# Kernel optimization log

Hardware: AMD Instinct MI355X
Metric: run time of the kernel (lower is better)

The kernel has to match this reference:

```python
import jax, jax.numpy as jnp
import numpy as np

IN_DIM, OUT_DIM, HID = 32, 1, 256
H0, H1, H2 = HID // 4, HID // 2, HID
B, S = 256, 512


def setup_inputs() -> dict:
    key = jax.random.key(0)
    ks = jax.random.split(key, 16)

    def u(k, shape, fan):
        bound = 1.0 / np.sqrt(fan)
        return jax.random.uniform(k, shape, jnp.float32, -bound, bound)

    inp = {"noise": jax.random.normal(ks[0], (B, S, IN_DIM), jnp.float32)}
    dims = [(IN_DIM, H0), (H0, H1), (H1, H2)]
    for i, (din, h) in enumerate(dims):
        inp[f"Wih{i}"] = u(ks[1 + 4 * i], (4 * h, din), h)  # torch gate order i,f,g,o
        inp[f"Whh{i}"] = u(ks[2 + 4 * i], (4 * h, h), h)
        inp[f"bih{i}"] = u(ks[3 + 4 * i], (4 * h,), h)
        inp[f"bhh{i}"] = u(ks[4 + 4 * i], (4 * h,), h)
    inp["Wl"] = u(ks[13], (OUT_DIM, H2), H2)
    inp["bl"] = u(ks[14], (OUT_DIM,), H2)
    return inp


def lstm_layer(x, Wih, Whh, bih, bhh):
    # x: [B, S, D] -> hidden sequence [B, S, H]; zero initial (h, c), torch gate order i,f,g,o
    Bb = x.shape[0]
    H = Whh.shape[1]
    pre = jnp.einsum('bsd,gd->bsg', x, Wih) + bih + bhh  # input GEMM for all timesteps at once

    def step(carry, pre_t):
        h, c = carry
        g = pre_t + h @ Whh.T  # [B, 4H]
        i, f, gg, o = jnp.split(g, 4, axis=-1)
        c = jax.nn.sigmoid(f) * c + jax.nn.sigmoid(i) * jnp.tanh(gg)
        h = jax.nn.sigmoid(o) * jnp.tanh(c)
        return (h, c), h

    h0 = jnp.zeros((Bb, H), x.dtype)
    c0 = jnp.zeros((Bb, H), x.dtype)
    _, hs = jax.lax.scan(step, (h0, c0), jnp.swapaxes(pre, 0, 1))  # scan over time
    return jnp.swapaxes(hs, 0, 1)


def reference(noise, Wih0, Whh0, bih0, bhh0, Wih1, Whh1, bih1, bhh1,
              Wih2, Whh2, bih2, bhh2, Wl, bl):
    x = lstm_layer(noise, Wih0, Whh0, bih0, bhh0)   # [B, S, 64]
    x = lstm_layer(x, Wih1, Whh1, bih1, bhh1)        # [B, S, 128]
    x = lstm_layer(x, Wih2, Whh2, bih2, bhh2)        # [B, S, 256]
    return jnp.tanh(jnp.einsum('bsh,oh->bso', x, Wl) + bl)  # [B, S, OUT_DIM]
```

## Files before the change

kernel.cpp:

```cpp
#include <hip/hip_runtime.h>
#include <hip/hip_fp16.h>

#define DEVINL __device__ __forceinline__

constexpr int B = 256, S = 512;
constexpr int H0 = 64, H1 = 128, H2 = 256;

typedef _Float16 f16x8 __attribute__((ext_vector_type(8)));
typedef float f32x4 __attribute__((ext_vector_type(4)));
typedef _Float16 h2v __attribute__((ext_vector_type(2)));

DEVINL float fexp2(float x) { return __builtin_amdgcn_exp2f(x); }
DEVINL float frcp(float x) { return __builtin_amdgcn_rcpf(x); }
DEVINL float fsig(float x) { return frcp(1.f + fexp2(-1.44269504088896f * x)); }
DEVINL float ftanh_(float x) { return 1.f - 2.f * frcp(1.f + fexp2(2.88539008177793f * x)); }
DEVINL h2v as_h2(unsigned u) { union { unsigned u; h2v h; } x; x.u = u; return x.h; }
DEVINL float fdot2(unsigned a, unsigned b, float c) {
  return __builtin_amdgcn_fdot2(as_h2(a), as_h2(b), c, false);
}
union FU { uint4 u; f16x8 h; };
DEVINL f16x8 as_f16x8(uint4 u) { FU x; x.u = u; return x.h; }

DEVINL unsigned long long agldull(unsigned long long* p) {
  return __hip_atomic_load(p, __ATOMIC_RELAXED, __HIP_MEMORY_SCOPE_AGENT);
}
DEVINL void agstull(unsigned long long* p, unsigned long long v) {
  __hip_atomic_store(p, v, __ATOMIC_RELAXED, __HIP_MEMORY_SCOPE_AGENT);
}


__global__ __launch_bounds__(256) void pack_frag(const float* __restrict__ w,
    uint4* __restrict__ wp, int Hch, int Kdim, int MT, int KT) {
  int o = blockIdx.x * 256 + threadIdx.x;
  if (o >= MT * KT * 64) return;
  int lane = o & 63, fk = o >> 6;
  int kt = fk % KT, mt = fk / KT;
  int rp = mt * 16 + (lane & 15);
  int orig = (rp & 3) * Hch + (rp >> 2);
  int k0 = kt * 32 + (lane >> 4) * 8;
  unsigned r[4];
#pragma unroll
  for (int p = 0; p < 4; ++p) {
    unsigned lo = __half_as_ushort(__float2half_rn(w[(size_t)orig * Kdim + k0 + 2 * p]));
    unsigned hi = __half_as_ushort(__float2half_rn(w[(size_t)orig * Kdim + k0 + 2 * p + 1]));
    r[p] = lo | (hi << 16);
  }
  uint4 v; v.x = r[0]; v.y = r[1]; v.z = r[2]; v.w = r[3];
  wp[o] = v;
}

__global__ __launch_bounds__(256) void pack_bias(const float* __restrict__ bih,
    const float* __restrict__ bhh, float* __restrict__ bs, int Hch) {
  int rp = blockIdx.x * 256 + threadIdx.x;
  if (rp >= 4 * Hch) return;
  int orig = (rp & 3) * Hch + (rp >> 2);
  bs[rp] = bih[orig] + bhh[orig];
}

__global__ void pack_wl(const float* __restrict__ wl, unsigned* __restrict__ wlp, int n) {
  int i = threadIdx.x;
  if (i < n) {
    unsigned lo = __half_as_ushort(__float2half_rn(wl[2 * i]));
    unsigned hi = __half_as_ushort(__float2half_rn(wl[2 * i + 1]));
    wlp[i] = lo | (hi << 16);
  }
}

__global__ __launch_bounds__(256) void f2h(const float* __restrict__ x,
                                           __half* __restrict__ y, int n8) {
  int i = blockIdx.x * 256 + threadIdx.x;
  if (i >= n8) return;
  float4 a = *(const float4*)(x + i * 8);
  float4 b = *(const float4*)(x + i * 8 + 4);
  __half h[8];
  h[0] = __float2half_rn(a.x); h[1] = __float2half_rn(a.y);
  h[2] = __float2half_rn(a.z); h[3] = __float2half_rn(a.w);
  h[4] = __float2half_rn(b.x); h[5] = __float2half_rn(b.y);
  h[6] = __float2half_rn(b.z); h[7] = __float2half_rn(b.w);
  *(uint4*)(y + i * 8) = *(const uint4*)h;
}

#define KBLK(BUF, K0, K1)                                                           \
  _Pragma("unroll") for (int kt = (K0); kt < (K1); ++kt) {                          \
    f16x8 bfrag = as_f16x8(*(const uint4*)((BUF) + n16 * HP + kt * 32 + quad * 8)); \
    _Pragma("unroll") for (int im = 0; im < MTW; ++im)                              \
      acc[im] = __builtin_amdgcn_mfma_f32_16x16x32_f16(                             \
          as_f16x8(areg[im][kt]), bfrag, acc[im], 0, 0, 0);                         \
  }

template <int H, int SPLIT, bool FINAL, int KTI>
DEVINL void scan_body(
    int bx, const __half* x, const uint4* wpI, const float* bs,
    const uint4* wp, f32x4* preT, __half* xout, float* out,
    const unsigned* wlp, const float* blp,
    float* sth, float* stc, unsigned long long* xh,
    int Sc, int t0, int first) {
  constexpr int MT = H / 4;
  constexpr int MTO = MT / SPLIT;
  constexpr int MTW = MTO / 8;
  constexpr int KT = H / 32;
  constexpr int HP = H + 8;
  constexpr int CH_OWN = MTO * 4;

  __shared__ __half hb[2][16 * HP];
  __shared__ unsigned wls[FINAL ? H / 2 : 1];

  const int tid = threadIdx.x, w = tid >> 6, lane = tid & 63;
  const int n16 = lane & 15, quad = lane >> 4;
  int bt, half;
  if constexpr (SPLIT == 2) { bt = bx & 15; half = bx >> 4; }
  else { bt = bx; half = 0; }
  const int b0 = bt * 16;
  const int mbase = half * MTO;

  {
    constexpr int KI = KTI * 32;
    uint4 wih[MTW][KTI];
#pragma unroll
    for (int im = 0; im < MTW; ++im)
#pragma unroll
      for (int kt = 0; kt < KTI; ++kt)
        wih[im][kt] = wpI[((size_t)(mbase + w * MTW + im) * KTI + kt) * 64 + lane];
    f32x4 bini[MTW];
#pragma unroll
    for (int im = 0; im < MTW; ++im)
      bini[im] = *(const f32x4*)(bs + (mbase + w * MTW + im) * 16 + quad * 4);
    uint4 bfr[KTI];
    {
      const __half* xr = x + ((size_t)(b0 + n16) * S + t0) * KI + quad * 8;
#pragma unroll
      for (int kt = 0; kt < KTI; ++kt) bfr[kt] = *(const uint4*)(xr + kt * 32);
    }
    for (int t = 0; t < Sc; ++t) {
      uint4 cur[KTI];
#pragma unroll
      for (int kt = 0; kt < KTI; ++kt) cur[kt] = bfr[kt];
      if (t + 1 < Sc) {
        const __half* xr = x + ((size_t)(b0 + n16) * S + t0 + t + 1) * KI + quad * 8;
#pragma unroll
        for (int kt = 0; kt < KTI; ++kt) bfr[kt] = *(const uint4*)(xr + kt * 32);
      }
      f32x4 ac[MTW];
#pragma unroll
      for (int im = 0; im < MTW; ++im) ac[im] = bini[im];
#pragma unroll
      for (int kt = 0; kt < KTI; ++kt)
#pragma unroll
        for (int im = 0; im < MTW; ++im)
          ac[im] = __builtin_amdgcn_mfma_f32_16x16x32_f16(as_f16x8(wih[im][kt]),
                                                          as_f16x8(cur[kt]), ac[im], 0, 0, 0);
#pragma unroll
      for (int im = 0; im < MTW; ++im)
        preT[((size_t)(bt * Sc + t) * MT + mbase + w * MTW + im) * 64 + lane] = ac[im];
    }
  }
  asm volatile("s_waitcnt vmcnt(0)" ::: "memory");

  uint4 areg[MTW][KT];
#pragma unroll
  for (int im = 0; im < MTW; ++im)
#pragma unroll
    for (int kt = 0; kt < KT; ++kt)
      areg[im][kt] = wp[((size_t)(mbase + w * MTW + im) * KT + kt) * 64 + lane];

  if constexpr (FINAL)
    for (int i = tid; i < H / 2; i += 512) wls[i] = wlp[i];

  float cst[MTW];
#pragma unroll
  for (int im = 0; im < MTW; ++im) {
    int ch = (mbase + w * MTW + im) * 4 + quad;
    cst[im] = first ? 0.f : stc[(size_t)(b0 + n16) * H + ch];
  }
  for (int i = tid; i < 16 * H; i += 512) {
    int n = i / H, ch = i % H;
    hb[0][n * HP + ch] = first ? __float2half_rn(0.f)
                               : __float2half_rn(sth[(size_t)(b0 + n) * H + ch]);
  }
  __syncthreads();

  const float bl0 = FINAL ? blp[0] : 0.f;

  auto emit_out = [&](const __half* rbuf, int t_out) {
    if constexpr (FINAL) {
      if ((SPLIT == 1 || half == 0) && tid < 128) {
        int n = tid >> 3, seg = tid & 7;
        const unsigned* hrow = (const unsigned*)(rbuf + n * HP);
        float s = 0.f;
#pragma unroll
        for (int p = 0; p < 16; ++p) s = fdot2(hrow[seg * 16 + p], wls[seg * 16 + p], s);
        s += __shfl_xor(s, 1); s += __shfl_xor(s, 2); s += __shfl_xor(s, 4);
        if (seg == 0) out[(size_t)(b0 + n) * S + t_out] = ftanh_(s + bl0);
      }
    } else {
      if (tid < 16 * (H / 8)) {
        int n = tid / (H / 8), kq = tid % (H / 8);
        uint4 v = *(const uint4*)(rbuf + n * HP + kq * 8);
        *(uint4*)(xout + ((size_t)(b0 + n) * S + t_out) * H + kq * 8) = v;
      }
    }
  };

  f32x4 nxt[MTW];
#pragma unroll
  for (int im = 0; im < MTW; ++im)
    nxt[im] = preT[((size_t)(bt * Sc) * MT + mbase + w * MTW + im) * 64 + lane];

  for (int tl = 0; tl < Sc; ++tl) {
    __half* rb = hb[tl & 1];
    __half* wb = hb[(tl + 1) & 1];
    f32x4 acc[MTW];
#pragma unroll
    for (int im = 0; im < MTW; ++im) acc[im] = nxt[im];
    if (tl + 1 < Sc) {
#pragma unroll
      for (int im = 0; im < MTW; ++im)
        nxt[im] = preT[((size_t)(bt * Sc + tl + 1) * MT + mbase + w * MTW + im) * 64 + lane];
    }

    if constexpr (SPLIT == 2) {
      unsigned long long v0 = 0, v1 = 0;
      unsigned long long* src = nullptr;
      const unsigned seq = (unsigned)(t0 + tl);
      const int j0 = w * 128 + lane;
      if (tl > 0) {
        src = xh + (((size_t)((t0 + tl - 1) & 1) * 16 + bt) * 2 + (1 - half)) * 1024;
        v0 = agldull(src + j0);
        v1 = agldull(src + j0 + 64);
      }
      if (half == 0) { KBLK(rb, 0, KT / 2) } else { KBLK(rb, KT / 2, KT) }
      if (tl > 0) {
        for (;;) {
          bool ok = ((unsigned)(v0 >> 32) == seq) & ((unsigned)(v1 >> 32) == seq);
          if (__all(ok)) break;
          __builtin_amdgcn_s_sleep(1);
          v0 = agldull(src + j0);
          v1 = agldull(src + j0 + 64);
        }
        int c0 = j0 >> 3, dn0 = j0 & 7;
        rb[(2 * dn0) * HP + (1 - half) * CH_OWN + c0] =
            __ushort_as_half((unsigned short)(v0 & 0xffffu));
        rb[(2 * dn0 + 1) * HP + (1 - half) * CH_OWN + c0] =
            __ushort_as_half((unsigned short)((v0 >> 16) & 0xffffu));
        int j1 = j0 + 64, c1 = j1 >> 3, dn1 = j1 & 7;
        rb[(2 * dn1) * HP + (1 - half) * CH_OWN + c1] =
            __ushort_as_half((unsigned short)(v1 & 0xffffu));
        rb[(2 * dn1 + 1) * HP + (1 - half) * CH_OWN + c1] =
            __ushort_as_half((unsigned short)((v1 >> 16) & 0xffffu));
        __syncthreads();
      }
      if (half == 0) { KBLK(rb, KT / 2, KT) } else { KBLK(rb, 0, KT / 2) }
      if (tl > 0) emit_out(rb, t0 + tl - 1);
    } else {
      if (tl > 0) emit_out(rb, t0 + tl - 1);
      KBLK(rb, 0, KT)
    }

    __half hh[MTW];
#pragma unroll
    for (int im = 0; im < MTW; ++im) {
      float gi = fsig(acc[im][0]);
      float gf = fsig(acc[im][1]);
      float gg = ftanh_(acc[im][2]);
      float go = fsig(acc[im][3]);
      float cn = gf * cst[im] + gi * gg;
      cst[im] = cn;
      hh[im] = __float2half_rn(go * ftanh_(cn));
    }

    if constexpr (SPLIT == 2) {
      const int hid = t0 + tl;
      const unsigned eseq = (unsigned)(hid + 1);
      unsigned long long* dst =
          xh + (((size_t)(hid & 1) * 16 + bt) * 2 + half) * 1024;
#pragma unroll
      for (int im = 0; im < MTW; ++im) {
        unsigned m = (unsigned)__half_as_ushort(hh[im]);
        unsigned o = (unsigned)__shfl_xor((int)m, 1);
        if (!(lane & 1)) {
          int cl = (w * MTW + im) * 4 + quad;
          agstull(dst + cl * 8 + (n16 >> 1),
                  ((unsigned long long)eseq << 32) | (unsigned long long)(m | (o << 16)));
        }
      }
#pragma unroll
      for (int im = 0; im < MTW; ++im)
        wb[n16 * HP + (mbase + w * MTW + im) * 4 + quad] = hh[im];
      __syncthreads();
    } else {
#pragma unroll
      for (int im = 0; im < MTW; ++im)
        wb[n16 * HP + (mbase + w * MTW + im) * 4 + quad] = hh[im];
      __syncthreads();
    }
  }

  __half* fb = hb[Sc & 1];
  if constexpr (SPLIT == 2) {
    const unsigned seq = (unsigned)(t0 + Sc);
    unsigned long long* src =
        xh + (((size_t)((t0 + Sc - 1) & 1) * 16 + bt) * 2 + (1 - half)) * 1024;
    const int j0 = w * 128 + lane;
    unsigned long long v0 = agldull(src + j0), v1 = agldull(src + j0 + 64);
    for (;;) {
      bool ok = ((unsigned)(v0 >> 32) == seq) & ((unsigned)(v1 >> 32) == seq);
      if (__all(ok)) break;
      __builtin_amdgcn_s_sleep(1);
      v0 = agldull(src + j0);
      v1 = agldull(src + j0 + 64);
    }
    int c0 = j0 >> 3, dn0 = j0 & 7;
    fb[(2 * dn0) * HP + (1 - half) * CH_OWN + c0] =
        __ushort_as_half((unsigned short)(v0 & 0xffffu));
    fb[(2 * dn0 + 1) * HP + (1 - half) * CH_OWN + c0] =
        __ushort_as_half((unsigned short)((v0 >> 16) & 0xffffu));
    int j1 = j0 + 64, c1 = j1 >> 3, dn1 = j1 & 7;
    fb[(2 * dn1) * HP + (1 - half) * CH_OWN + c1] =
        __ushort_as_half((unsigned short)(v1 & 0xffffu));
    fb[(2 * dn1 + 1) * HP + (1 - half) * CH_OWN + c1] =
        __ushort_as_half((unsigned short)((v1 >> 16) & 0xffffu));
    __syncthreads();
  }

  emit_out(fb, t0 + Sc - 1);

  for (int i = tid; i < 16 * H; i += 512) {
    int n = i / H, ch = i % H;
    sth[(size_t)(b0 + n) * H + ch] = __half2float(fb[n * HP + ch]);
  }
#pragma unroll
  for (int im = 0; im < MTW; ++im) {
    int ch = (mbase + w * MTW + im) * 4 + quad;
    stc[(size_t)(b0 + n16) * H + ch] = cst[im];
  }
}
#undef KBLK

__global__ __launch_bounds__(512) void scan_fat(
    const __half* x0, __half* x1, __half* x2,
    const uint4* wpI0, const uint4* wpI1, const uint4* wpI2,
    const float* bs0, const float* bs1, const float* bs2,
    const uint4* wpH0, const uint4* wpH1, const uint4* wpH2,
    f32x4* preT0, f32x4* preT1, f32x4* preT2,
    float* out, const unsigned* wlp, const float* blp,
    float* sh0, float* sc0, float* sh1, float* sc1, float* sh2, float* sc2,
    unsigned long long* xh, int Sc, int slot, int NC) {
  int b = blockIdx.x;
  if (b < 16) {
    int c = slot;
    if (c >= NC) return;
    scan_body<64, 1, false, 1>(b, x0, wpI0, bs0, wpH0, preT0, x1, nullptr,
                               nullptr, nullptr, sh0, sc0, nullptr, Sc, c * Sc, c == 0);
  } else if (b < 32) {
    int c = slot - 1;
    if (c < 0 || c >= NC) return;
    scan_body<128, 1, false, 2>(b - 16, x1, wpI1, bs1, wpH1, preT1, x2, nullptr,
                                nullptr, nullptr, sh1, sc1, nullptr, Sc, c * Sc, c == 0);
  } else {
    int c = slot - 2;
    if (c < 0 || c >= NC) return;
    scan_body<256, 2, true, 4>(b - 32, x2, wpI2, bs2, wpH2, preT2, nullptr, out,
                               wlp, blp, sh2, sc2, xh, Sc, c * Sc, c == 0);
  }
}

extern "C" void kernel_launch(void* const* d_in, const int* in_sizes, int n_in,
                              void* d_out, int out_size, void* d_ws, size_t ws_size,
                              hipStream_t stream) {
  (void)in_sizes; (void)n_in; (void)out_size;
  const float* noise = (const float*)d_in[0];
  const float* Wih0 = (const float*)d_in[1];
  const float* Whh0 = (const float*)d_in[2];
  const float* bih0 = (const float*)d_in[3];
  const float* bhh0 = (const float*)d_in[4];
  const float* Wih1 = (const float*)d_in[5];
  const float* Whh1 = (const float*)d_in[6];
  const float* bih1 = (const float*)d_in[7];
  const float* bhh1 = (const float*)d_in[8];
  const float* Wih2 = (const float*)d_in[9];
  const float* Whh2 = (const float*)d_in[10];
  const float* bih2 = (const float*)d_in[11];
  const float* bhh2 = (const float*)d_in[12];
  const float* Wl = (const float*)d_in[13];
  const float* bl = (const float*)d_in[14];
  float* out = (float*)d_out;

  char* p = (char*)d_ws;
  auto alloc = [&](size_t bytes) {
    char* r = p;
    p += (bytes + 255) & ~(size_t)255;
    return r;
  };
  uint4* wpH0 = (uint4*)alloc((size_t)16 * 2 * 1024);
  uint4* wpH1 = (uint4*)alloc((size_t)32 * 4 * 1024);
  uint4* wpH2 = (uint4*)alloc((size_t)64 * 8 * 1024);
  uint4* wpI0 = (uint4*)alloc((size_t)16 * 1 * 1024);
  uint4* wpI1 = (uint4*)alloc((size_t)32 * 2 * 1024);
  uint4* wpI2 = (uint4*)alloc((size_t)64 * 4 * 1024);
  float* bs0 = (float*)alloc(256 * 4);
  float* bs1 = (float*)alloc(512 * 4);
  float* bs2 = (float*)alloc(1024 * 4);
  unsigned* wlp = (unsigned*)alloc(128 * 4);
  float* sh0 = (float*)alloc((size_t)B * H0 * 4);
  float* sc0 = (float*)alloc((size_t)B * H0 * 4);
  float* sh1 = (float*)alloc((size_t)B * H1 * 4);
  float* sc1 = (float*)alloc((size_t)B * H1 * 4);
  float* sh2 = (float*)alloc((size_t)B * H2 * 4);
  float* sc2 = (float*)alloc((size_t)B * H2 * 4);
  __half* x0 = (__half*)alloc((size_t)B * S * 32 * 2);
  __half* x1 = (__half*)alloc((size_t)B * S * H0 * 2);
  __half* x2 = (__half*)alloc((size_t)B * S * H1 * 2);
  unsigned long long* xh = (unsigned long long*)alloc((size_t)2 * 16 * 2 * 1024 * 8);
  size_t fixed = (size_t)(p - (char*)d_ws);
  int Sc = 64;
  while (Sc > 16 && fixed + (size_t)B * Sc * 16 * (H0 + H1 + H2) > ws_size) Sc >>= 1;
  f32x4* preT0 = (f32x4*)alloc((size_t)B * Sc * 16 * H0);
  f32x4* preT1 = (f32x4*)alloc((size_t)B * Sc * 16 * H1);
  f32x4* preT2 = (f32x4*)alloc((size_t)B * Sc * 16 * H2);

  hipMemsetAsync(xh, 0, (size_t)2 * 16 * 2 * 1024 * 8, stream);

  pack_frag<<<(16 * 2 * 64 + 255) / 256, 256, 0, stream>>>(Whh0, wpH0, 64, 64, 16, 2);
  pack_frag<<<(32 * 4 * 64 + 255) / 256, 256, 0, stream>>>(Whh1, wpH1, 128, 128, 32, 4);
  pack_frag<<<(64 * 8 * 64 + 255) / 256, 256, 0, stream>>>(Whh2, wpH2, 256, 256, 64, 8);
  pack_frag<<<(16 * 1 * 64 + 255) / 256, 256, 0, stream>>>(Wih0, wpI0, 64, 32, 16, 1);
  pack_frag<<<(32 * 2 * 64 + 255) / 256, 256, 0, stream>>>(Wih1, wpI1, 128, 64, 32, 2);
  pack_frag<<<(64 * 4 * 64 + 255) / 256, 256, 0, stream>>>(Wih2, wpI2, 256, 128, 64, 4);
  pack_bias<<<1, 256, 0, stream>>>(bih0, bhh0, bs0, 64);
  pack_bias<<<2, 256, 0, stream>>>(bih1, bhh1, bs1, 128);
  pack_bias<<<4, 256, 0, stream>>>(bih2, bhh2, bs2, 256);
  pack_wl<<<1, 128, 0, stream>>>(Wl, wlp, 128);
  f2h<<<(B * S * 32 / 8 + 255) / 256, 256, 0, stream>>>(noise, x0, B * S * 32 / 8);

  int NC = S / Sc;
  for (int slot = 0; slot < NC + 2; ++slot)
    scan_fat<<<64, 512, 0, stream>>>(x0, x1, x2, wpI0, wpI1, wpI2, bs0, bs1, bs2,
                                     wpH0, wpH1, wpH2, preT0, preT1, preT2,
                                     out, wlp, bl, sh0, sc0, sh1, sc1, sh2, sc2,
                                     xh, Sc, slot, NC);
}
```

Baseline: 1.907 ms.

## Exchange partial gate sums instead of hidden halves across split blocks

For the layer that is split over two blocks, each block now keeps only its half of the hidden state and computes partial gate products for the other block's rows. It exchanges these fp32 partial sums through global memory with sequence tags, so each block no longer has to rebuild the full hidden vector in shared memory. This is meant to remove a mid-step barrier and the shared-memory scatter from the recurrent critical path. The final output projection is also split into two partial dot products joined by a second handshake. In exchange, each step moves more data across blocks, keeps twice the weight fragments in registers, and adds more spin-wait traffic.

```diff
diff --git a/kernel.cpp b/kernel.cpp
--- a/kernel.cpp
+++ b/kernel.cpp
@@ -80,14 +80,6 @@
   *(uint4*)(y + i * 8) = *(const uint4*)h;
 }
 
-#define KBLK(BUF, K0, K1)                                                           \
-  _Pragma("unroll") for (int kt = (K0); kt < (K1); ++kt) {                          \
-    f16x8 bfrag = as_f16x8(*(const uint4*)((BUF) + n16 * HP + kt * 32 + quad * 8)); \
-    _Pragma("unroll") for (int im = 0; im < MTW; ++im)                              \
-      acc[im] = __builtin_amdgcn_mfma_f32_16x16x32_f16(                             \
-          as_f16x8(areg[im][kt]), bfrag, acc[im], 0, 0, 0);                         \
-  }
-
 template <int H, int SPLIT, bool FINAL, int KTI>
 DEVINL void scan_body(
     int bx, const __half* x, const uint4* wpI, const float* bs,
@@ -99,11 +91,13 @@
   constexpr int MTO = MT / SPLIT;
   constexpr int MTW = MTO / 8;
   constexpr int KT = H / 32;
-  constexpr int HP = H + 8;
-  constexpr int CH_OWN = MTO * 4;
+  constexpr int KTH = KT / SPLIT;
+  constexpr int HLOC = H / SPLIT;
+  constexpr int HP = HLOC + 8;
+  constexpr int XSLOT = MTW * 4 * 512;
 
   __shared__ __half hb[2][16 * HP];
-  __shared__ unsigned wls[FINAL ? H / 2 : 1];
+  __shared__ unsigned wls[FINAL ? (HLOC / 2) : 1];
 
   const int tid = threadIdx.x, w = tid >> 6, lane = tid & 63;
   const int n16 = lane & 15, quad = lane >> 4;
@@ -112,6 +106,7 @@
   else { bt = bx; half = 0; }
   const int b0 = bt * 16;
   const int mbase = half * MTO;
+  unsigned long long* dxh = xh + (size_t)2 * 16 * 2 * XSLOT;
 
   {
     constexpr int KI = KTI * 32;
@@ -156,15 +151,25 @@
   }
   asm volatile("s_waitcnt vmcnt(0)" ::: "memory");
 
-  uint4 areg[MTW][KT];
+  uint4 aregO[MTW][KTH];
 #pragma unroll
   for (int im = 0; im < MTW; ++im)
 #pragma unroll
-    for (int kt = 0; kt < KT; ++kt)
-      areg[im][kt] = wp[((size_t)(mbase + w * MTW + im) * KT + kt) * 64 + lane];
+    for (int kt = 0; kt < KTH; ++kt)
+      aregO[im][kt] =
+          wp[((size_t)(mbase + w * MTW + im) * KT + half * KTH + kt) * 64 + lane];
+  uint4 aregC[SPLIT == 2 ? MTW : 1][SPLIT == 2 ? KTH : 1];
+  if constexpr (SPLIT == 2) {
+#pragma unroll
+    for (int im = 0; im < MTW; ++im)
+#pragma unroll
+      for (int kt = 0; kt < KTH; ++kt)
+        aregC[im][kt] =
+            wp[((size_t)((1 - half) * MTO + w * MTW + im) * KT + half * KTH + kt) * 64 + lane];
+  }
 
   if constexpr (FINAL)
-    for (int i = tid; i < H / 2; i += 512) wls[i] = wlp[i];
+    for (int i = tid; i < HLOC / 2; i += 512) wls[i] = wlp[half * (HLOC / 2) + i];
 
   float cst[MTW];
 #pragma unroll
@@ -172,34 +177,15 @@
     int ch = (mbase + w * MTW + im) * 4 + quad;
     cst[im] = first ? 0.f : stc[(size_t)(b0 + n16) * H + ch];
   }
-  for (int i = tid; i < 16 * H; i += 512) {
-    int n = i / H, ch = i % H;
-    hb[0][n * HP + ch] = first ? __float2half_rn(0.f)
-                               : __float2half_rn(sth[(size_t)(b0 + n) * H + ch]);
+  for (int i = tid; i < 16 * HLOC; i += 512) {
+    int n = i / HLOC, chl = i % HLOC;
+    hb[0][n * HP + chl] =
+        first ? __float2half_rn(0.f)
+              : __float2half_rn(sth[(size_t)(b0 + n) * H + half * HLOC + chl]);
   }
   __syncthreads();
 
   const float bl0 = FINAL ? blp[0] : 0.f;
-
-  auto emit_out = [&](const __half* rbuf, int t_out) {
-    if constexpr (FINAL) {
-      if ((SPLIT == 1 || half == 0) && tid < 128) {
-        int n = tid >> 3, seg = tid & 7;
-        const unsigned* hrow = (const unsigned*)(rbuf + n * HP);
-        float s = 0.f;
-#pragma unroll
-        for (int p = 0; p < 16; ++p) s = fdot2(hrow[seg * 16 + p], wls[seg * 16 + p], s);
-        s += __shfl_xor(s, 1); s += __shfl_xor(s, 2); s += __shfl_xor(s, 4);
-        if (seg == 0) out[(size_t)(b0 + n) * S + t_out] = ftanh_(s + bl0);
-      }
-    } else {
-      if (tid < 16 * (H / 8)) {
-        int n = tid / (H / 8), kq = tid % (H / 8);
-        uint4 v = *(const uint4*)(rbuf + n * HP + kq * 8);
-        *(uint4*)(xout + ((size_t)(b0 + n) * S + t_out) * H + kq * 8) = v;
-      }
-    }
-  };
 
   f32x4 nxt[MTW];
 #pragma unroll
@@ -209,6 +195,8 @@
   for (int tl = 0; tl < Sc; ++tl) {
     __half* rb = hb[tl & 1];
     __half* wb = hb[(tl + 1) & 1];
+    const int hid = t0 + tl;
+    const unsigned seq = (unsigned)(hid + 1);
     f32x4 acc[MTW];
 #pragma unroll
     for (int im = 0; im < MTW; ++im) acc[im] = nxt[im];
@@ -218,42 +206,97 @@
         nxt[im] = preT[((size_t)(bt * Sc + tl + 1) * MT + mbase + w * MTW + im) * 64 + lane];
     }
 
+    unsigned long long v[SPLIT == 2 ? MTW : 1][SPLIT == 2 ? 4 : 1];
+    unsigned long long* src = nullptr;
+    float sOwn = 0.f;
+    unsigned long long vdot = 0ull;
+
     if constexpr (SPLIT == 2) {
-      unsigned long long v0 = 0, v1 = 0;
-      unsigned long long* src = nullptr;
-      const unsigned seq = (unsigned)(t0 + tl);
-      const int j0 = w * 128 + lane;
+      f32x4 accc[MTW];
+#pragma unroll
+      for (int im = 0; im < MTW; ++im) accc[im] = f32x4{0.f, 0.f, 0.f, 0.f};
+#pragma unroll
+      for (int kt = 0; kt < KTH; ++kt) {
+        f16x8 bf = as_f16x8(*(const uint4*)(rb + n16 * HP + kt * 32 + quad * 8));
+#pragma unroll
+        for (int im = 0; im < MTW; ++im)
+          accc[im] = __builtin_amdgcn_mfma_f32_16x16x32_f16(as_f16x8(aregC[im][kt]), bf,
+                                                            accc[im], 0, 0, 0);
+      }
+      unsigned long long* dst =
+          xh + (((size_t)(hid & 1) * 16 + bt) * 2 + half) * XSLOT;
+#pragma unroll
+      for (int im = 0; im < MTW; ++im)
+#pragma unroll
+        for (int g = 0; g < 4; ++g)
+          agstull(dst + (im * 4 + g) * 512 + w * 64 + lane,
+                  ((unsigned long long)seq << 32) |
+                      (unsigned long long)__float_as_uint(accc[im][g]));
+      src = xh + (((size_t)(hid & 1) * 16 + bt) * 2 + (1 - half)) * XSLOT;
+#pragma unroll
+      for (int im = 0; im < MTW; ++im)
+#pragma unroll
+        for (int g = 0; g < 4; ++g)
+          v[im][g] = agldull(src + (im * 4 + g) * 512 + w * 64 + lane);
+
+      if constexpr (FINAL) {
+        if (tl > 0 && w == 0) {
+          const int b = lane >> 2, q = lane & 3;
+          const unsigned* hrow = (const unsigned*)(rb + b * HP);
+          float s = 0.f;
+#pragma unroll
+          for (int p = 0; p < 16; ++p) s = fdot2(hrow[q * 16 + p], wls[q * 16 + p], s);
+          s += __shfl_xor(s, 1); s += __shfl_xor(s, 2);
+          sOwn = s;
+          unsigned long long* dbase = dxh + ((size_t)((hid - 1) & 1) * 16 + bt) * 16;
+          if (half == 1) {
+            if (q == 0)
+              agstull(dbase + b, ((unsigned long long)(unsigned)hid << 32) |
+                                     (unsigned long long)__float_as_uint(s));
+          } else {
+            if (q == 0) vdot = agldull(dbase + b);
+          }
+        }
+      }
+    }
+
+#pragma unroll
+    for (int kt = 0; kt < KTH; ++kt) {
+      f16x8 bf = as_f16x8(*(const uint4*)(rb + n16 * HP + kt * 32 + quad * 8));
+#pragma unroll
+      for (int im = 0; im < MTW; ++im)
+        acc[im] = __builtin_amdgcn_mfma_f32_16x16x32_f16(as_f16x8(aregO[im][kt]), bf,
+                                                         acc[im], 0, 0, 0);
+    }
+
+    if constexpr (SPLIT == 2) {
+      for (;;) {
+        bool ok = true;
+#pragma unroll
+        for (int im = 0; im < MTW; ++im)
+#pragma unroll
+          for (int g = 0; g < 4; ++g) ok &= ((unsigned)(v[im][g] >> 32) == seq);
+        if (__all(ok)) break;
+        __builtin_amdgcn_s_sleep(1);
+#pragma unroll
+        for (int im = 0; im < MTW; ++im)
+#pragma unroll
+          for (int g = 0; g < 4; ++g)
+            v[im][g] = agldull(src + (im * 4 + g) * 512 + w * 64 + lane);
+      }
+#pragma unroll
+      for (int im = 0; im < MTW; ++im)
+#pragma unroll
+        for (int g = 0; g < 4; ++g)
+          acc[im][g] += __uint_as_float((unsigned)v[im][g]);
+    } else {
       if (tl > 0) {
-        src = xh + (((size_t)((t0 + tl - 1) & 1) * 16 + bt) * 2 + (1 - half)) * 1024;
-        v0 = agldull(src + j0);
-        v1 = agldull(src + j0 + 64);
-      }
-      if (half == 0) { KBLK(rb, 0, KT / 2) } else { KBLK(rb, KT / 2, KT) }
-      if (tl > 0) {
-        for (;;) {
-          bool ok = ((unsigned)(v0 >> 32) == seq) & ((unsigned)(v1 >> 32) == seq);
-          if (__all(ok)) break;
-          __builtin_amdgcn_s_sleep(1);
-          v0 = agldull(src + j0);
-          v1 = agldull(src + j0 + 64);
+        if (tid < 16 * (H / 8)) {
+          int n = tid / (H / 8), kq = tid % (H / 8);
+          uint4 vv = *(const uint4*)(rb + n * HP + kq * 8);
+          *(uint4*)(xout + ((size_t)(b0 + n) * S + t0 + tl - 1) * H + kq * 8) = vv;
         }
-        int c0 = j0 >> 3, dn0 = j0 & 7;
-        rb[(2 * dn0) * HP + (1 - half) * CH_OWN + c0] =
-            __ushort_as_half((unsigned short)(v0 & 0xffffu));
-        rb[(2 * dn0 + 1) * HP + (1 - half) * CH_OWN + c0] =
-            __ushort_as_half((unsigned short)((v0 >> 16) & 0xffffu));
-        int j1 = j0 + 64, c1 = j1 >> 3, dn1 = j1 & 7;
-        rb[(2 * dn1) * HP + (1 - half) * CH_OWN + c1] =
-            __ushort_as_half((unsigned short)(v1 & 0xffffu));
-        rb[(2 * dn1 + 1) * HP + (1 - half) * CH_OWN + c1] =
-            __ushort_as_half((unsigned short)((v1 >> 16) & 0xffffu));
-        __syncthreads();
-      }
-      if (half == 0) { KBLK(rb, KT / 2, KT) } else { KBLK(rb, 0, KT / 2) }
-      if (tl > 0) emit_out(rb, t0 + tl - 1);
-    } else {
-      if (tl > 0) emit_out(rb, t0 + tl - 1);
-      KBLK(rb, 0, KT)
+      }
     }
 
     __half hh[MTW];
@@ -267,66 +310,72 @@
       cst[im] = cn;
       hh[im] = __float2half_rn(go * ftanh_(cn));
     }
-
-    if constexpr (SPLIT == 2) {
-      const int hid = t0 + tl;
-      const unsigned eseq = (unsigned)(hid + 1);
-      unsigned long long* dst =
-          xh + (((size_t)(hid & 1) * 16 + bt) * 2 + half) * 1024;
-#pragma unroll
-      for (int im = 0; im < MTW; ++im) {
-        unsigned m = (unsigned)__half_as_ushort(hh[im]);
-        unsigned o = (unsigned)__shfl_xor((int)m, 1);
-        if (!(lane & 1)) {
-          int cl = (w * MTW + im) * 4 + quad;
-          agstull(dst + cl * 8 + (n16 >> 1),
-                  ((unsigned long long)eseq << 32) | (unsigned long long)(m | (o << 16)));
+#pragma unroll
+    for (int im = 0; im < MTW; ++im)
+      wb[n16 * HP + (w * MTW + im) * 4 + quad] = hh[im];
+
+    if constexpr (SPLIT == 2 && FINAL) {
+      if (tl > 0 && w == 0 && half == 0) {
+        const int b = lane >> 2, q = lane & 3;
+        unsigned long long* dbase = dxh + ((size_t)((hid - 1) & 1) * 16 + bt) * 16;
+        for (;;) {
+          bool ok = (q != 0) || ((unsigned)(vdot >> 32) == (unsigned)hid);
+          if (__all(ok)) break;
+          __builtin_amdgcn_s_sleep(1);
+          if (q == 0) vdot = agldull(dbase + b);
         }
-      }
-#pragma unroll
-      for (int im = 0; im < MTW; ++im)
-        wb[n16 * HP + (mbase + w * MTW + im) * 4 + quad] = hh[im];
-      __syncthreads();
-    } else {
-#pragma unroll
-      for (int im = 0; im < MTW; ++im)
-        wb[n16 * HP + (mbase + w * MTW + im) * 4 + quad] = hh[im];
-      __syncthreads();
-    }
+        if (q == 0)
+          out[(size_t)(b0 + b) * S + (hid - 1)] =
+              ftanh_(sOwn + __uint_as_float((unsigned)vdot) + bl0);
+      }
+    }
+
+    __syncthreads();
   }
 
   __half* fb = hb[Sc & 1];
+
   if constexpr (SPLIT == 2) {
-    const unsigned seq = (unsigned)(t0 + Sc);
-    unsigned long long* src =
-        xh + (((size_t)((t0 + Sc - 1) & 1) * 16 + bt) * 2 + (1 - half)) * 1024;
-    const int j0 = w * 128 + lane;
-    unsigned long long v0 = agldull(src + j0), v1 = agldull(src + j0 + 64);
-    for (;;) {
-      bool ok = ((unsigned)(v0 >> 32) == seq) & ((unsigned)(v1 >> 32) == seq);
-      if (__all(ok)) break;
-      __builtin_amdgcn_s_sleep(1);
-      v0 = agldull(src + j0);
-      v1 = agldull(src + j0 + 64);
-    }
-    int c0 = j0 >> 3, dn0 = j0 & 7;
-    fb[(2 * dn0) * HP + (1 - half) * CH_OWN + c0] =
-        __ushort_as_half((unsigned short)(v0 & 0xffffu));
-    fb[(2 * dn0 + 1) * HP + (1 - half) * CH_OWN + c0] =
-        __ushort_as_half((unsigned short)((v0 >> 16) & 0xffffu));
-    int j1 = j0 + 64, c1 = j1 >> 3, dn1 = j1 & 7;
-    fb[(2 * dn1) * HP + (1 - half) * CH_OWN + c1] =
-        __ushort_as_half((unsigned short)(v1 & 0xffffu));
-    fb[(2 * dn1 + 1) * HP + (1 - half) * CH_OWN + c1] =
-        __ushort_as_half((unsigned short)((v1 >> 16) & 0xffffu));
-    __syncthreads();
-  }
-
-  emit_out(fb, t0 + Sc - 1);
-
-  for (int i = tid; i < 16 * H; i += 512) {
-    int n = i / H, ch = i % H;
-    sth[(size_t)(b0 + n) * H + ch] = __half2float(fb[n * HP + ch]);
+    if constexpr (FINAL) {
+      const int tlast = t0 + Sc - 1;
+      if (w == 0) {
+        const int b = lane >> 2, q = lane & 3;
+        const unsigned* hrow = (const unsigned*)(fb + b * HP);
+        float s = 0.f;
+#pragma unroll
+        for (int p = 0; p < 16; ++p) s = fdot2(hrow[q * 16 + p], wls[q * 16 + p], s);
+        s += __shfl_xor(s, 1); s += __shfl_xor(s, 2);
+        unsigned long long* dbase = dxh + ((size_t)(tlast & 1) * 16 + bt) * 16;
+        if (half == 1) {
+          if (q == 0)
+            agstull(dbase + b, ((unsigned long long)(unsigned)(tlast + 1) << 32) |
+                                   (unsigned long long)__float_as_uint(s));
+        } else {
+          unsigned long long vd = 0ull;
+          if (q == 0) vd = agldull(dbase + b);
+          for (;;) {
+            bool ok = (q != 0) || ((unsigned)(vd >> 32) == (unsigned)(tlast + 1));
+            if (__all(ok)) break;
+            __builtin_amdgcn_s_sleep(1);
+            if (q == 0) vd = agldull(dbase + b);
+          }
+          if (q == 0)
+            out[(size_t)(b0 + b) * S + tlast] =
+                ftanh_(s + __uint_as_float((unsigned)vd) + bl0);
+        }
+      }
+    }
+  } else {
+    if (tid < 16 * (H / 8)) {
+      int n = tid / (H / 8), kq = tid % (H / 8);
+      uint4 vv = *(const uint4*)(fb + n * HP + kq * 8);
+      *(uint4*)(xout + ((size_t)(b0 + n) * S + t0 + Sc - 1) * H + kq * 8) = vv;
+    }
+  }
+
+  for (int i = tid; i < 16 * HLOC; i += 512) {
+    int n = i / HLOC, chl = i % HLOC;
+    sth[(size_t)(b0 + n) * H + half * HLOC + chl] = __half2float(fb[n * HP + chl]);
   }
 #pragma unroll
   for (int im = 0; im < MTW; ++im) {
@@ -334,7 +383,6 @@
     stc[(size_t)(b0 + n16) * H + ch] = cst[im];
   }
 }
-#undef KBLK
 
 __global__ __launch_bounds__(512) void scan_fat(
     const __half* x0, __half* x1, __half* x2,
@@ -410,7 +458,8 @@
   __half* x0 = (__half*)alloc((size_t)B * S * 32 * 2);
   __half* x1 = (__half*)alloc((size_t)B * S * H0 * 2);
   __half* x2 = (__half*)alloc((size_t)B * S * H1 * 2);
-  unsigned long long* xh = (unsigned long long*)alloc((size_t)2 * 16 * 2 * 1024 * 8);
+  const size_t XH_ULL = (size_t)2 * 16 * 2 * 8192 + (size_t)2 * 16 * 16;
+  unsigned long long* xh = (unsigned long long*)alloc(XH_ULL * 8);
   size_t fixed = (size_t)(p - (char*)d_ws);
   int Sc = 64;
   while (Sc > 16 && fixed + (size_t)B * Sc * 16 * (H0 + H1 + H2) > ws_size) Sc >>= 1;
@@ -418,7 +467,7 @@
   f32x4* preT1 = (f32x4*)alloc((size_t)B * Sc * 16 * H1);
   f32x4* preT2 = (f32x4*)alloc((size_t)B * Sc * 16 * H2);
 
-  hipMemsetAsync(xh, 0, (size_t)2 * 16 * 2 * 1024 * 8, stream);
+  hipMemsetAsync(xh, 0, XH_ULL * 8, stream);
 
   pack_frag<<<(16 * 2 * 64 + 255) / 256, 256, 0, stream>>>(Whh0, wpH0, 64, 64, 16, 2);
   pack_frag<<<(32 * 4 * 64 + 255) / 256, 256, 0, stream>>>(Whh1, wpH1, 128, 128, 32, 4);
```

New measurement: 3.635 ms. +90.7%, slower.

## Fuse input projection into recurrent step for layers 0 and 1, drop preT buffers

Applied to the files above, without the earlier changes.

For the unsplit layers (H=64,128), the input-projection MFMAs now run inside each recurrent timestep, with the next x row prefetched in registers. This removes the separate pre-pass that wrote the preT0/preT1 buffers and the per-step reads of them. The layer-2 cross-block exchange now issues the peer's handshake load right after publishing its own h, and the s_sleep is dropped from the spin loop. The cost is more register pressure and more MFMA work on the serial critical path of layers 0 and 1, and tighter spinning in layer 2.

```diff
diff --git a/kernel.cpp b/kernel.cpp
--- a/kernel.cpp
+++ b/kernel.cpp
@@ -101,6 +101,7 @@
   constexpr int KT = H / 32;
   constexpr int HP = H + 8;
   constexpr int CH_OWN = MTO * 4;
+  constexpr int KI = KTI * 32;
 
   __shared__ __half hb[2][16 * HP];
   __shared__ unsigned wls[FINAL ? H / 2 : 1];
@@ -113,8 +114,7 @@
   const int b0 = bt * 16;
   const int mbase = half * MTO;
 
-  {
-    constexpr int KI = KTI * 32;
+  if constexpr (SPLIT == 2) {
     uint4 wih[MTW][KTI];
 #pragma unroll
     for (int im = 0; im < MTW; ++im)
@@ -153,8 +153,21 @@
       for (int im = 0; im < MTW; ++im)
         preT[((size_t)(bt * Sc + t) * MT + mbase + w * MTW + im) * 64 + lane] = ac[im];
     }
-  }
-  asm volatile("s_waitcnt vmcnt(0)" ::: "memory");
+    asm volatile("s_waitcnt vmcnt(0)" ::: "memory");
+  }
+
+  uint4 wih1[SPLIT == 1 ? MTW : 1][SPLIT == 1 ? KTI : 1];
+  f32x4 bini1[SPLIT == 1 ? MTW : 1];
+  if constexpr (SPLIT == 1) {
+#pragma unroll
+    for (int im = 0; im < MTW; ++im)
+#pragma unroll
+      for (int kt = 0; kt < KTI; ++kt)
+        wih1[im][kt] = wpI[((size_t)(w * MTW + im) * KTI + kt) * 64 + lane];
+#pragma unroll
+    for (int im = 0; im < MTW; ++im)
+      bini1[im] = *(const f32x4*)(bs + (w * MTW + im) * 16 + quad * 4);
+  }
 
   uint4 areg[MTW][KT];
 #pragma unroll
@@ -202,40 +215,46 @@
   };
 
   f32x4 nxt[MTW];
-#pragma unroll
-  for (int im = 0; im < MTW; ++im)
-    nxt[im] = preT[((size_t)(bt * Sc) * MT + mbase + w * MTW + im) * 64 + lane];
+  if constexpr (SPLIT == 2) {
+#pragma unroll
+    for (int im = 0; im < MTW; ++im)
+      nxt[im] = preT[((size_t)(bt * Sc) * MT + mbase + w * MTW + im) * 64 + lane];
+  }
+  uint4 xcur[SPLIT == 1 ? KTI : 1];
+  if constexpr (SPLIT == 1) {
+    const __half* xr = x + ((size_t)(b0 + n16) * S + t0) * KI + quad * 8;
+#pragma unroll
+    for (int kt = 0; kt < KTI; ++kt) xcur[kt] = *(const uint4*)(xr + kt * 32);
+  }
+
+  unsigned long long v0 = 0, v1 = 0;
+  const int j0 = w * 128 + lane;
 
   for (int tl = 0; tl < Sc; ++tl) {
     __half* rb = hb[tl & 1];
     __half* wb = hb[(tl + 1) & 1];
+    const int hid = t0 + tl;
     f32x4 acc[MTW];
-#pragma unroll
-    for (int im = 0; im < MTW; ++im) acc[im] = nxt[im];
-    if (tl + 1 < Sc) {
-#pragma unroll
-      for (int im = 0; im < MTW; ++im)
-        nxt[im] = preT[((size_t)(bt * Sc + tl + 1) * MT + mbase + w * MTW + im) * 64 + lane];
-    }
 
     if constexpr (SPLIT == 2) {
-      unsigned long long v0 = 0, v1 = 0;
-      unsigned long long* src = nullptr;
-      const unsigned seq = (unsigned)(t0 + tl);
-      const int j0 = w * 128 + lane;
-      if (tl > 0) {
-        src = xh + (((size_t)((t0 + tl - 1) & 1) * 16 + bt) * 2 + (1 - half)) * 1024;
-        v0 = agldull(src + j0);
-        v1 = agldull(src + j0 + 64);
-      }
+#pragma unroll
+      for (int im = 0; im < MTW; ++im) acc[im] = nxt[im];
+      if (tl + 1 < Sc) {
+#pragma unroll
+        for (int im = 0; im < MTW; ++im)
+          nxt[im] = preT[((size_t)(bt * Sc + tl + 1) * MT + mbase + w * MTW + im) * 64 + lane];
+      }
+
       if (half == 0) { KBLK(rb, 0, KT / 2) } else { KBLK(rb, KT / 2, KT) }
       if (tl > 0) {
+        const unsigned seq = (unsigned)hid;
+        unsigned long long* srcp =
+            xh + (((size_t)((hid - 1) & 1) * 16 + bt) * 2 + (1 - half)) * 1024;
         for (;;) {
           bool ok = ((unsigned)(v0 >> 32) == seq) & ((unsigned)(v1 >> 32) == seq);
           if (__all(ok)) break;
-          __builtin_amdgcn_s_sleep(1);
-          v0 = agldull(src + j0);
-          v1 = agldull(src + j0 + 64);
+          v0 = agldull(srcp + j0);
+          v1 = agldull(srcp + j0 + 64);
         }
         int c0 = j0 >> 3, dn0 = j0 & 7;
         rb[(2 * dn0) * HP + (1 - half) * CH_OWN + c0] =
@@ -250,10 +269,28 @@
         __syncthreads();
       }
       if (half == 0) { KBLK(rb, KT / 2, KT) } else { KBLK(rb, 0, KT / 2) }
-      if (tl > 0) emit_out(rb, t0 + tl - 1);
+      if (tl > 0) emit_out(rb, hid - 1);
     } else {
-      if (tl > 0) emit_out(rb, t0 + tl - 1);
+      uint4 xnxt[KTI];
+      if (tl + 1 < Sc) {
+        const __half* xr = x + ((size_t)(b0 + n16) * S + hid + 1) * KI + quad * 8;
+#pragma unroll
+        for (int kt = 0; kt < KTI; ++kt) xnxt[kt] = *(const uint4*)(xr + kt * 32);
+      }
+#pragma unroll
+      for (int im = 0; im < MTW; ++im) acc[im] = bini1[im];
+#pragma unroll
+      for (int kt = 0; kt < KTI; ++kt)
+#pragma unroll
+        for (int im = 0; im < MTW; ++im)
+          acc[im] = __builtin_amdgcn_mfma_f32_16x16x32_f16(as_f16x8(wih1[im][kt]),
+                                                           as_f16x8(xcur[kt]), acc[im], 0, 0, 0);
+      if (tl > 0) emit_out(rb, hid - 1);
       KBLK(rb, 0, KT)
+      if (tl + 1 < Sc) {
+#pragma unroll
+        for (int kt = 0; kt < KTI; ++kt) xcur[kt] = xnxt[kt];
+      }
     }
 
     __half hh[MTW];
@@ -269,7 +306,6 @@
     }
 
     if constexpr (SPLIT == 2) {
-      const int hid = t0 + tl;
       const unsigned eseq = (unsigned)(hid + 1);
       unsigned long long* dst =
           xh + (((size_t)(hid & 1) * 16 + bt) * 2 + half) * 1024;
@@ -283,6 +319,12 @@
                   ((unsigned long long)eseq << 32) | (unsigned long long)(m | (o << 16)));
         }
       }
+      {
+        unsigned long long* srcn =
+            xh + (((size_t)(hid & 1) * 16 + bt) * 2 + (1 - half)) * 1024;
+        v0 = agldull(srcn + j0);
+        v1 = agldull(srcn + j0 + 64);
+      }
 #pragma unroll
       for (int im = 0; im < MTW; ++im)
         wb[n16 * HP + (mbase + w * MTW + im) * 4 + quad] = hh[im];
@@ -290,7 +332,7 @@
     } else {
 #pragma unroll
       for (int im = 0; im < MTW; ++im)
-        wb[n16 * HP + (mbase + w * MTW + im) * 4 + quad] = hh[im];
+        wb[n16 * HP + (w * MTW + im) * 4 + quad] = hh[im];
       __syncthreads();
     }
   }
@@ -298,16 +340,13 @@
   __half* fb = hb[Sc & 1];
   if constexpr (SPLIT == 2) {
     const unsigned seq = (unsigned)(t0 + Sc);
-    unsigned long long* src =
+    unsigned long long* srcp =
         xh + (((size_t)((t0 + Sc - 1) & 1) * 16 + bt) * 2 + (1 - half)) * 1024;
-    const int j0 = w * 128 + lane;
-    unsigned long long v0 = agldull(src + j0), v1 = agldull(src + j0 + 64);
     for (;;) {
       bool ok = ((unsigned)(v0 >> 32) == seq) & ((unsigned)(v1 >> 32) == seq);
       if (__all(ok)) break;
-      __builtin_amdgcn_s_sleep(1);
-      v0 = agldull(src + j0);
-      v1 = agldull(src + j0 + 64);
+      v0 = agldull(srcp + j0);
+      v1 = agldull(srcp + j0 + 64);
     }
     int c0 = j0 >> 3, dn0 = j0 & 7;
     fb[(2 * dn0) * HP + (1 - half) * CH_OWN + c0] =
@@ -341,7 +380,7 @@
     const uint4* wpI0, const uint4* wpI1, const uint4* wpI2,
     const float* bs0, const float* bs1, const float* bs2,
     const uint4* wpH0, const uint4* wpH1, const uint4* wpH2,
-    f32x4* preT0, f32x4* preT1, f32x4* preT2,
+    f32x4* preT2,
     float* out, const unsigned* wlp, const float* blp,
     float* sh0, float* sc0, float* sh1, float* sc1, float* sh2, float* sc2,
     unsigned long long* xh, int Sc, int slot, int NC) {
@@ -349,12 +388,12 @@
   if (b < 16) {
     int c = slot;
     if (c >= NC) return;
-    scan_body<64, 1, false, 1>(b, x0, wpI0, bs0, wpH0, preT0, x1, nullptr,
+    scan_body<64, 1, false, 1>(b, x0, wpI0, bs0, wpH0, nullptr, x1, nullptr,
                                nullptr, nullptr, sh0, sc0, nullptr, Sc, c * Sc, c == 0);
   } else if (b < 32) {
     int c = slot - 1;
     if (c < 0 || c >= NC) return;
-    scan_body<128, 1, false, 2>(b - 16, x1, wpI1, bs1, wpH1, preT1, x2, nullptr,
+    scan_body<128, 1, false, 2>(b - 16, x1, wpI1, bs1, wpH1, nullptr, x2, nullptr,
                                 nullptr, nullptr, sh1, sc1, nullptr, Sc, c * Sc, c == 0);
   } else {
     int c = slot - 2;
@@ -413,9 +452,7 @@
   unsigned long long* xh = (unsigned long long*)alloc((size_t)2 * 16 * 2 * 1024 * 8);
   size_t fixed = (size_t)(p - (char*)d_ws);
   int Sc = 64;
-  while (Sc > 16 && fixed + (size_t)B * Sc * 16 * (H0 + H1 + H2) > ws_size) Sc >>= 1;
-  f32x4* preT0 = (f32x4*)alloc((size_t)B * Sc * 16 * H0);
-  f32x4* preT1 = (f32x4*)alloc((size_t)B * Sc * 16 * H1);
+  while (Sc > 16 && fixed + (size_t)B * Sc * 16 * H2 > ws_size) Sc >>= 1;
   f32x4* preT2 = (f32x4*)alloc((size_t)B * Sc * 16 * H2);
 
   hipMemsetAsync(xh, 0, (size_t)2 * 16 * 2 * 1024 * 8, stream);
@@ -435,7 +472,7 @@
   int NC = S / Sc;
   for (int slot = 0; slot < NC + 2; ++slot)
     scan_fat<<<64, 512, 0, stream>>>(x0, x1, x2, wpI0, wpI1, wpI2, bs0, bs1, bs2,
-                                     wpH0, wpH1, wpH2, preT0, preT1, preT2,
+                                     wpH0, wpH1, wpH2, preT2,
                                      out, wlp, bl, sh0, sc0, sh1, sc1, sh2, sc2,
                                      xh, Sc, slot, NC);
 }
```

After: 1.924 ms. Within noise of the previous version (+0.9%).
